# Optimization experiments

Hardware: AMD Instinct MI355X
Metric: run time of the kernel (lower is better)

Reference implementation:

```python
import jax, jax.numpy as jnp
import numpy as np

HEADS = 5 - 1  # 4 attention heads (GPSConv heads=4)


def _bn(x, g, b, eps=1e-5):
    # BatchNorm1d, training-mode math (biased variance), matches torch normalization
    mu = x.mean(0)
    var = x.var(0)
    return g * (x - mu) * jax.lax.rsqrt(var + eps) + b


def _forward(x, t, freqs, t_fc1_W, t_fc1_b, t_fc2_W, t_fc2_b, node_W, node_b,
             tproj_W, tproj_b, tcat_W, tcat_b, pen_g, pen_b, pel_W, pel_b,
             cat_W, cat_b, conv_Wg, gru_Wih, gru_bih, gru_Whh, gru_bhh,
             attn_Wqkv, attn_bqkv, attn_Wo, attn_bo, bn_g, bn_b,
             mlp_W1, mlp_b1, mlp_W2, mlp_b2, out_W, out_b):
    B, C, Hh, Ww = x.shape
    HD = node_W.shape[1]          # hidden_dim = 64
    DH = HD // HEADS              # per-head dim = 16
    WL = pen_g.shape[0]           # walk_length = 20

    xf = x.reshape(B, -1)                              # [B, D]
    h = xf @ node_W + node_b                           # node_proj

    # TimeEmbedding: t @ freqs -> sin/cos -> MLP, then time_proj
    tp = t.reshape(B, 1) * freqs.reshape(1, -1)        # [B, nf]
    two_pi = jnp.asarray(2.0 * np.pi, x.dtype)
    te = jnp.concatenate([jnp.sin(two_pi * tp), jnp.cos(two_pi * tp)], axis=-1)
    te = jax.nn.silu(te @ t_fc1_W + t_fc1_b) @ t_fc2_W + t_fc2_b
    h_time = te @ tproj_W + tproj_b
    h = jnp.concatenate([h, h_time], axis=-1) @ tcat_W + tcat_b  # time_cat_proj

    # Fully-connected graph incl. self-loops: A = 1 everywhere, deg = B.
    # Random-walk PE: P = A/deg has all entries 1/B; P is idempotent (P@P = P),
    # hence diag(P^k) = diag(P) = 1/B for every k in 1..walk_length.
    A = jnp.ones((B, B), x.dtype)
    P = A / A.sum(1, keepdims=True)
    pe = jnp.broadcast_to(jnp.diagonal(P)[:, None], (B, WL))
    pe = _bn(pe, pen_g, pen_b)                         # pe_norm (batch stats)
    h = jnp.concatenate([h, pe @ pel_W + pel_b], axis=-1) @ cat_W + cat_b

    inv_sqrt = jnp.asarray(1.0 / np.sqrt(DH), x.dtype)
    for l in range(conv_Wg.shape[0]):                  # 5 GPSConv layers
        # --- GatedGraphConv (num_layers=1): message, add-aggregate, GRU ---
        m = A @ (h @ conv_Wg[l])                       # sum of messages from all src nodes
        gi = m @ gru_Wih[l] + gru_bih[l]               # [B, 3H]
        gh = h @ gru_Whh[l] + gru_bhh[l]
        ir, iz, inn = jnp.split(gi, 3, axis=-1)
        hr, hz, hn = jnp.split(gh, 3, axis=-1)
        r = jax.nn.sigmoid(ir + hr)
        z = jax.nn.sigmoid(iz + hz)
        n = jnp.tanh(inn + r * hn)
        hc = (1.0 - z) * n + z * h                     # GRUCell output
        h1 = _bn(hc + h, bn_g[l, 0], bn_b[l, 0])       # residual + norm1

        # --- global multihead self-attention over the single dense batch ---
        qkv = h @ attn_Wqkv[l] + attn_bqkv[l]
        q, k, v = jnp.split(qkv, 3, axis=-1)
        q = q.reshape(B, HEADS, DH).transpose(1, 0, 2)  # [h, B, d]
        k = k.reshape(B, HEADS, DH).transpose(1, 0, 2)
        v = v.reshape(B, HEADS, DH).transpose(1, 0, 2)
        att = jax.nn.softmax(jnp.einsum('hqd,hkd->hqk', q, k) * inv_sqrt, axis=-1)
        o = jnp.einsum('hqk,hkd->hqd', att, v).transpose(1, 0, 2).reshape(B, HD)
        o = o @ attn_Wo[l] + attn_bo[l]
        h2 = _bn(o + h, bn_g[l, 1], bn_b[l, 1])        # residual + norm2

        s = h1 + h2
        s = s + (jax.nn.relu(s @ mlp_W1[l] + mlp_b1[l]) @ mlp_W2[l] + mlp_b2[l])
        h = _bn(s, bn_g[l, 2], bn_b[l, 2])             # norm3

    return (h @ out_W + out_b).reshape(B, C, Hh, Ww)


def setup_inputs() -> dict:
    key = jax.random.key(0)
    B, C, H, W = 2048, 4, 32, 32
    D = C * H * W                 # 4096
    HD, PE, WL, L = 64, 16, 20, 5
    NF, TH, TC = 8, 64, 64
    ks = iter(jax.random.split(key, 40))

    def rn(shape, s=0.05):
        return jax.random.normal(next(ks), shape, jnp.float32) * s

    return {
        'x': jax.random.normal(next(ks), (B, C, H, W), jnp.float32),
        't': jax.random.uniform(next(ks), (B,), jnp.float32),
        'freqs': rn((NF,), 1.0),
        't_fc1_W': rn((2 * NF, TH)), 't_fc1_b': rn((TH,)),
        't_fc2_W': rn((TH, TC)), 't_fc2_b': rn((TC,)),
        'node_W': rn((D, HD), 0.02), 'node_b': rn((HD,)),
        'tproj_W': rn((TC, HD)), 'tproj_b': rn((HD,)),
        'tcat_W': rn((2 * HD, HD)), 'tcat_b': rn((HD,)),
        'pen_g': jnp.ones((WL,), jnp.float32), 'pen_b': jnp.zeros((WL,), jnp.float32),
        'pel_W': rn((WL, PE)), 'pel_b': rn((PE,)),
        'cat_W': rn((HD + PE, HD)), 'cat_b': rn((HD,)),
        'conv_Wg': rn((L, HD, HD)),
        'gru_Wih': rn((L, HD, 3 * HD)), 'gru_bih': rn((L, 3 * HD)),
        'gru_Whh': rn((L, HD, 3 * HD)), 'gru_bhh': rn((L, 3 * HD)),
        'attn_Wqkv': rn((L, HD, 3 * HD)), 'attn_bqkv': rn((L, 3 * HD)),
        'attn_Wo': rn((L, HD, HD)), 'attn_bo': rn((L, HD)),
        'bn_g': jnp.ones((L, 3, HD), jnp.float32), 'bn_b': jnp.zeros((L, 3, HD), jnp.float32),
        'mlp_W1': rn((L, HD, 2 * HD)), 'mlp_b1': rn((L, 2 * HD)),
        'mlp_W2': rn((L, 2 * HD, HD)), 'mlp_b2': rn((L, HD)),
        'out_W': rn((HD, D)), 'out_b': rn((D,)),
    }


def reference(x, t, freqs, t_fc1_W, t_fc1_b, t_fc2_W, t_fc2_b, node_W, node_b,
              tproj_W, tproj_b, tcat_W, tcat_b, pen_g, pen_b, pel_W, pel_b,
              cat_W, cat_b, conv_Wg, gru_Wih, gru_bih, gru_Whh, gru_bhh,
              attn_Wqkv, attn_bqkv, attn_Wo, attn_bo, bn_g, bn_b,
              mlp_W1, mlp_b1, mlp_W2, mlp_b2, out_W, out_b):
    return _forward(x, t, freqs, t_fc1_W, t_fc1_b, t_fc2_W, t_fc2_b, node_W, node_b,
                    tproj_W, tproj_b, tcat_W, tcat_b, pen_g, pen_b, pel_W, pel_b,
                    cat_W, cat_b, conv_Wg, gru_Wih, gru_bih, gru_Whh, gru_bhh,
                    attn_Wqkv, attn_bqkv, attn_Wo, attn_bo, bn_g, bn_b,
                    mlp_W1, mlp_b1, mlp_W2, mlp_b2, out_W, out_b)
```

## Files before the change

kernel.cpp:

```cpp
#include <hip/hip_runtime.h>

#define NB 2048
#define HDM 64
#define NLAY 5

typedef __bf16 bf16x8 __attribute__((ext_vector_type(8)));
typedef float v4f __attribute__((ext_vector_type(4)));

__device__ __forceinline__ float sigmoidf_(float x){ return 1.f/(1.f+__expf(-x)); }
__device__ __forceinline__ float tanhfast_(float x){
  x = fminf(fmaxf(x, -15.f), 15.f);
  float e = __expf(2.f*x);
  return (e-1.f)/(e+1.f);
}
__device__ __forceinline__ unsigned short f2b_rne(float f){
  unsigned u = __float_as_uint(f);
  unsigned r = u + 0x7FFFu + ((u>>16)&1u);
  return (unsigned short)(r>>16);
}
__device__ __forceinline__ unsigned pk2(float a, float b){
  unsigned ua = (__float_as_uint(a) + 0x8000u) >> 16;
  unsigned ub = (__float_as_uint(b) + 0x8000u) & 0xFFFF0000u;
  return ua | ub;
}

__global__ __launch_bounds__(256) void k_pre(
    const float* __restrict__ x, const float* __restrict__ tt,
    const float* __restrict__ freqs,
    const float* __restrict__ fc1W, const float* __restrict__ fc1b,
    const float* __restrict__ fc2W, const float* __restrict__ fc2b,
    const float* __restrict__ tprojW, const float* __restrict__ tprojb,
    const float* __restrict__ nodeW,
    float* __restrict__ h0p, float* __restrict__ htime,
    float* __restrict__ zero_region)
{
  __shared__ float xs[16*256];
  __shared__ float tb0[256];
  __shared__ float tb1[256];
  const int t = threadIdx.x, blk = blockIdx.x;
  const int r = t>>6, c = t&63;

  if (blk == 0){
    for (int i = t; i < 320 + 1920; i += 256) zero_region[i] = 0.f;
  }

  {
    const int row = blk*4 + r;
    const float tv = tt[row];
    float te[16];
    #pragma unroll
    for (int j=0;j<8;++j){
      float sv, cv;
      __sincosf(6.28318530717958647692f*tv*freqs[j], &sv, &cv);
      te[j]=sv; te[j+8]=cv;
    }
    float a = fc1b[c];
    #pragma unroll
    for (int j=0;j<16;++j) a += te[j]*fc1W[j*64+c];
    tb0[t] = a*sigmoidf_(a);
    __syncthreads();
    float b2 = fc2b[c];
    for (int k=0;k<64;++k) b2 += tb0[r*64+k]*fc2W[k*64+c];
    tb1[t] = b2;
    __syncthreads();
    float hti = tprojb[c];
    for (int k=0;k<64;++k) hti += tb1[r*64+k]*tprojW[k*64+c];
    htime[row*64+c] = hti;
  }

  const int rg = blk>>2, kq = blk&3;
  const int rows0 = rg*16, k0 = kq*1024;
  const int cq = t&15, rr = t>>4;
  float4 acc; acc.x=0.f; acc.y=0.f; acc.z=0.f; acc.w=0.f;
  for (int ch=0; ch<4; ++ch){
    __syncthreads();
    const int kb = k0 + ch*256;
    #pragma unroll
    for (int i=0;i<4;++i){
      int fi = t + 256*i;
      int xr = fi>>6, kk = (fi&63)<<2;
      *(float4*)&xs[xr*256+kk] = *(const float4*)&x[(size_t)(rows0+xr)*4096 + kb + kk];
    }
    __syncthreads();
    #pragma unroll 4
    for (int k=0;k<256;++k){
      float4 w = *(const float4*)&nodeW[(size_t)(kb+k)*64 + 4*cq];
      float xv = xs[rr*256+k];
      acc.x += xv*w.x; acc.y += xv*w.y; acc.z += xv*w.z; acc.w += xv*w.w;
    }
  }
  *(float4*)&h0p[(size_t)kq*(NB*HDM) + (rows0+rr)*64 + 4*cq] = acc;
}

__global__ __launch_bounds__(256) void k_assemble(
    const float* __restrict__ h0p, const float* __restrict__ htime,
    const float* __restrict__ nodeb,
    const float* __restrict__ tcatW, const float* __restrict__ tcatb,
    const float* __restrict__ penb, const float* __restrict__ pelW,
    const float* __restrict__ pelb,
    const float* __restrict__ catW, const float* __restrict__ catb,
    float* __restrict__ hbuf)
{
  __shared__ float sa[256];
  __shared__ float sb[256];
  __shared__ float cvec[64];
  const int t = threadIdx.x, blk = blockIdx.x;
  const int r = t>>6, c = t&63;
  const int row = blk*4 + r;

  if (r==0){
    float pl[16];
    #pragma unroll
    for (int j=0;j<16;++j){
      float a = pelb[j];
      for (int w=0;w<20;++w) a += penb[w]*pelW[w*16+j];
      pl[j]=a;
    }
    float a = catb[c];
    #pragma unroll
    for (int j=0;j<16;++j) a += pl[j]*catW[(64+j)*64+c];
    cvec[c]=a;
  }
  float h0 = nodeb[c];
  #pragma unroll
  for (int q=0;q<4;++q) h0 += h0p[(size_t)q*(NB*HDM) + row*64 + c];
  sa[t] = h0;
  sb[t] = htime[row*64+c];
  __syncthreads();
  float a = tcatb[c];
  for (int k=0;k<64;++k) a += sa[r*64+k]*tcatW[k*64+c];
  for (int k=0;k<64;++k) a += sb[r*64+k]*tcatW[(64+k)*64+c];
  __syncthreads();
  sa[t] = a;
  __syncthreads();
  float hv = cvec[c];
  for (int k=0;k<64;++k) hv += sa[r*64+k]*catW[k*64+c];
  hbuf[row*64+c] = hv;
}

__global__ __launch_bounds__(256) void k_A(
    const float* __restrict__ smlp,
    const float* __restrict__ bnaccPrev,
    const float* __restrict__ gPrev, const float* __restrict__ bPrev,
    float* __restrict__ hbuf, float* __restrict__ hsumL,
    const float* __restrict__ Whh, const float* __restrict__ bhh,
    const float* __restrict__ Wq,  const float* __restrict__ bq,
    float* __restrict__ gh,
    unsigned short* __restrict__ Qb, unsigned short* __restrict__ Kb,
    unsigned short* __restrict__ Vt, int first)
{
  __shared__ float sa[256];
  const int t = threadIdx.x, blk = blockIdx.x;
  const int r = t>>6, c = t&63;
  const int row0 = blk*4;
  const int row = row0 + r;

  float hv;
  if (first){
    hv = hbuf[row*64+c];
  } else {
    float mu = bnaccPrev[256+c]*(1.f/NB);
    float va = bnaccPrev[320+c]*(1.f/NB) - mu*mu;
    hv = gPrev[c]*(smlp[row*64+c]-mu)*rsqrtf(va+1e-5f)+bPrev[c];
    hbuf[row*64+c] = hv;
  }
  sa[t] = hv;
  __syncthreads();
  if (t<64){
    atomicAdd(&hsumL[t], sa[t]+sa[64+t]+sa[128+t]+sa[192+t]);
  }
  #pragma unroll
  for (int i=0;i<3;++i){
    int idx = t + 256*i;
    int rr = idx/192, cc = idx - rr*192;
    float ag = bhh[cc], aq = bq[cc];
    for (int k=0;k<64;++k){
      float hk = sa[rr*64+k];
      ag += hk*Whh[k*192+cc];
      aq += hk*Wq[k*192+cc];
    }
    int rw = row0+rr;
    gh[(size_t)rw*192+cc] = ag;
    if (cc < 64){
      int hd = cc>>4, dh = cc&15;
      size_t base = ((size_t)(hd<<11) + rw)*32;
      Qb[base+dh] = f2b_rne(aq*0.25f);
      Qb[base+16+dh] = 0;
    } else if (cc < 128){
      int c2 = cc-64, hd = c2>>4, dh = c2&15;
      size_t base = ((size_t)(hd<<11) + rw)*32;
      Kb[base+dh] = f2b_rne(aq);
      Kb[base+16+dh] = 0;
    } else {
      int c2 = cc-128, hd = c2>>4, dh = c2&15;
      Vt[((size_t)(hd*16+dh))*2048 + rw] = f2b_rne(aq);
    }
  }
}

__global__ __launch_bounds__(64) void k_attn(
    const unsigned short* __restrict__ Qb, const unsigned short* __restrict__ Kb,
    const unsigned short* __restrict__ Vt,
    float* __restrict__ Upart, float* __restrict__ mpart, float* __restrict__ lpart)
{
  __shared__ unsigned short Pl[16*40];
  const int lane = threadIdx.x;
  const int q15 = lane & 15, quad = lane >> 4;
  const int b = blockIdx.x;
  const int qt = b & 127, head = (b>>7)&3, part = b>>9;
  const int qrow = qt*16 + q15;
  const int key00 = part*512;

  const bf16x8 qf = *(const bf16x8*)&Qb[(((size_t)(head<<11))+qrow)*32 + quad*8];
  const unsigned short* Kb_h = Kb + ((size_t)(head<<11))*32;
  const unsigned short* Vrow = Vt + ((size_t)(head*16+q15))*2048;

  v4f O = {0.f,0.f,0.f,0.f};
  float m = -1e30f, lsum = 0.f;

  bf16x8 kf0 = *(const bf16x8*)&Kb_h[(size_t)(key00 + q15)*32 + quad*8];
  bf16x8 kf1 = *(const bf16x8*)&Kb_h[(size_t)(key00 + 16 + q15)*32 + quad*8];
  bf16x8 vf  = *(const bf16x8*)&Vrow[key00 + quad*8];

  for (int c=0; c<16; ++c){
    bf16x8 nk0, nk1, nv;
    if (c < 15){
      int nk = key00 + (c+1)*32;
      nk0 = *(const bf16x8*)&Kb_h[(size_t)(nk + q15)*32 + quad*8];
      nk1 = *(const bf16x8*)&Kb_h[(size_t)(nk + 16 + q15)*32 + quad*8];
      nv  = *(const bf16x8*)&Vrow[nk + quad*8];
    }
    v4f z = {0.f,0.f,0.f,0.f};
    v4f s0 = __builtin_amdgcn_mfma_f32_16x16x32_bf16(kf0, qf, z, 0,0,0);
    v4f s1 = __builtin_amdgcn_mfma_f32_16x16x32_bf16(kf1, qf, z, 0,0,0);
    float cmax = fmaxf(fmaxf(fmaxf(s0[0],s0[1]),fmaxf(s0[2],s0[3])),
                       fmaxf(fmaxf(s1[0],s1[1]),fmaxf(s1[2],s1[3])));
    cmax = fmaxf(cmax, __shfl_xor(cmax,16,64));
    cmax = fmaxf(cmax, __shfl_xor(cmax,32,64));
    float mnew = fmaxf(m, cmax);
    float alpha = __expf(m - mnew);
    float p0=__expf(s0[0]-mnew), p1=__expf(s0[1]-mnew), p2=__expf(s0[2]-mnew), p3=__expf(s0[3]-mnew);
    float p4=__expf(s1[0]-mnew), p5=__expf(s1[1]-mnew), p6=__expf(s1[2]-mnew), p7=__expf(s1[3]-mnew);
    lsum = alpha*lsum + ((p0+p1)+(p2+p3)+((p4+p5)+(p6+p7)));
    m = mnew;
    O[0]*=alpha; O[1]*=alpha; O[2]*=alpha; O[3]*=alpha;
    *(uint2*)&Pl[q15*40 + quad*4]      = make_uint2(pk2(p0,p1), pk2(p2,p3));
    *(uint2*)&Pl[q15*40 + 16 + quad*4] = make_uint2(pk2(p4,p5), pk2(p6,p7));
    __syncthreads();
    bf16x8 pf = *(const bf16x8*)&Pl[q15*40 + quad*8];
    O = __builtin_amdgcn_mfma_f32_16x16x32_bf16(vf, pf, O, 0,0,0);
    kf0 = nk0; kf1 = nk1; vf = nv;
  }
  lsum += __shfl_xor(lsum,16,64);
  lsum += __shfl_xor(lsum,32,64);
  size_t ub = ((size_t)((part*4+head)*2048) + qrow)*16 + quad*4;
  *(float4*)&Upart[ub] = make_float4(O[0],O[1],O[2],O[3]);
  if (quad==0){
    mpart[(size_t)(part*4+head)*2048 + qrow] = m;
    lpart[(size_t)(part*4+head)*2048 + qrow] = lsum;
  }
}

__global__ __launch_bounds__(256) void k_B2(
    const float* __restrict__ hbuf, const float* __restrict__ gh,
    const float* __restrict__ hsumL,
    const float* __restrict__ Upart, const float* __restrict__ mpart,
    const float* __restrict__ lpart,
    const float* __restrict__ Wg,   const float* __restrict__ Wih,
    const float* __restrict__ bih,  const float* __restrict__ Wo,
    const float* __restrict__ bo,
    float* __restrict__ s1, float* __restrict__ s2, float* __restrict__ bnaccL)
{
  __shared__ float sa[256];
  __shared__ float os[256];
  __shared__ float smv_[64];
  __shared__ float sgi[192];
  __shared__ float Sb[512];
  const int t = threadIdx.x, blk = blockIdx.x;
  const int r = t>>6, c = t&63;
  const int row = blk*4 + r;
  const int head = c>>4, dh = c&15;

  if (t<64){
    float a=0.f;
    for (int k=0;k<64;++k) a += hsumL[k]*Wg[k*64+t];
    smv_[t]=a;
  }
  sa[t] = hbuf[row*64+c];

  float m0 = mpart[(size_t)(head)*2048+row],    m1 = mpart[(size_t)(4+head)*2048+row];
  float m2 = mpart[(size_t)(8+head)*2048+row],  m3 = mpart[(size_t)(12+head)*2048+row];
  float mm = fmaxf(fmaxf(m0,m1),fmaxf(m2,m3));
  float a0=__expf(m0-mm), a1=__expf(m1-mm), a2=__expf(m2-mm), a3=__expf(m3-mm);
  float ll = a0*lpart[(size_t)(head)*2048+row]   + a1*lpart[(size_t)(4+head)*2048+row]
           + a2*lpart[(size_t)(8+head)*2048+row] + a3*lpart[(size_t)(12+head)*2048+row];
  float uu = a0*Upart[((size_t)(head)*2048+row)*16+dh]    + a1*Upart[((size_t)(4+head)*2048+row)*16+dh]
           + a2*Upart[((size_t)(8+head)*2048+row)*16+dh]  + a3*Upart[((size_t)(12+head)*2048+row)*16+dh];
  os[t] = uu / ll;
  __syncthreads();
  if (t<192){
    float a = bih[t];
    for (int k=0;k<64;++k) a += smv_[k]*Wih[k*192+t];
    sgi[t]=a;
  }
  __syncthreads();

  float o2 = bo[c];
  for (int k=0;k<64;++k) o2 += os[r*64+k]*Wo[k*64+c];
  float hv = sa[t];
  float s2v = o2 + hv;
  float ir = sgi[c]      + gh[(size_t)row*192+c];
  float iz = sgi[64+c]   + gh[(size_t)row*192+64+c];
  float inn = sgi[128+c];
  float hn  = gh[(size_t)row*192+128+c];
  float rr_ = sigmoidf_(ir);
  float zz  = sigmoidf_(iz);
  float nn  = tanhfast_(inn + rr_*hn);
  float s1v = (1.f-zz)*nn + zz*hv + hv;
  s1[row*64+c] = s1v;
  s2[row*64+c] = s2v;
  Sb[t] = s1v; Sb[256+t] = s2v;
  __syncthreads();
  if (t<64){
    float a=0.f,aq=0.f,b=0.f,bq2=0.f;
    #pragma unroll
    for (int rr=0;rr<4;++rr){
      float v1 = Sb[rr*64+t], v2 = Sb[256+rr*64+t];
      a+=v1; aq+=v1*v1; b+=v2; bq2+=v2*v2;
    }
    atomicAdd(&bnaccL[t],a);     atomicAdd(&bnaccL[64+t],aq);
    atomicAdd(&bnaccL[128+t],b); atomicAdd(&bnaccL[192+t],bq2);
  }
}

__global__ __launch_bounds__(256) void k_C(
    const float* __restrict__ s1, const float* __restrict__ s2,
    const float* __restrict__ bngL, const float* __restrict__ bnbL,
    const float* __restrict__ W1, const float* __restrict__ b1,
    const float* __restrict__ W2, const float* __restrict__ b2,
    float* __restrict__ smlp, float* __restrict__ bnaccL)
{
  __shared__ float sa[256];
  __shared__ float sh[512];
  __shared__ float S2[256];
  const int t = threadIdx.x, blk = blockIdx.x;
  const int r = t>>6, c = t&63;
  const int row = blk*4 + r;

  float mu1 = bnaccL[c]*(1.f/NB);
  float va1 = bnaccL[64+c]*(1.f/NB) - mu1*mu1;
  float mu2 = bnaccL[128+c]*(1.f/NB);
  float va2 = bnaccL[192+c]*(1.f/NB) - mu2*mu2;
  float h1 = bngL[c]*(s1[row*64+c]-mu1)*rsqrtf(va1+1e-5f)+bnbL[c];
  float h2 = bngL[64+c]*(s2[row*64+c]-mu2)*rsqrtf(va2+1e-5f)+bnbL[64+c];
  float sv = h1+h2;
  sa[t]=sv;
  __syncthreads();
  #pragma unroll
  for (int i=0;i<2;++i){
    int idx = t + 256*i;
    int rr = idx>>7, hj = idx&127;
    float a = b1[hj];
    for (int k=0;k<64;++k) a += sa[rr*64+k]*W1[k*128+hj];
    sh[idx] = fmaxf(a, 0.f);
  }
  __syncthreads();
  float mo = b2[c];
  for (int k=0;k<128;++k) mo += sh[r*128+k]*W2[k*64+c];
  float smv2 = sv + mo;
  smlp[row*64+c]=smv2;
  S2[t]=smv2;
  __syncthreads();
  if (t<64){
    float a=0.f,aq=0.f;
    #pragma unroll
    for (int rr=0;rr<4;++rr){ float v=S2[rr*64+t]; a+=v; aq+=v*v; }
    atomicAdd(&bnaccL[256+t],a); atomicAdd(&bnaccL[320+t],aq);
  }
}

__global__ __launch_bounds__(256) void k_out(
  const float* __restrict__ smlp, const float* __restrict__ bnacc4,
  const float* __restrict__ g4, const float* __restrict__ b4,
  const float* __restrict__ outW, const float* __restrict__ outb,
  float* __restrict__ out)
{
  __shared__ float hsT[64*20];
  const int t = threadIdx.x, blk = blockIdx.x;
  const int rg = blk>>2, cg = blk&3;
  const int rows0 = rg*16;
  #pragma unroll
  for (int i=0;i<4;++i){
    int idx = t + 256*i;
    int k = idx&63, rr = idx>>6;
    float mu = bnacc4[256+k]*(1.f/NB);
    float va = bnacc4[320+k]*(1.f/NB)-mu*mu;
    hsT[k*20+rr] = g4[k]*(smlp[(size_t)(rows0+rr)*64+k]-mu)*rsqrtf(va+1e-5f)+b4[k];
  }
  __syncthreads();
  for (int j=0;j<4;++j){
    int cc = cg*1024 + t + 256*j;
    float acc[16];
    float bv = outb[cc];
    #pragma unroll
    for (int rr=0;rr<16;++rr) acc[rr]=bv;
    for (int k=0;k<64;++k){
      float w = outW[(size_t)k*4096+cc];
      const float4* hp = (const float4*)&hsT[k*20];
      float4 h0=hp[0], h1=hp[1], h2=hp[2], h3=hp[3];
      acc[0]+=h0.x*w;  acc[1]+=h0.y*w;  acc[2]+=h0.z*w;  acc[3]+=h0.w*w;
      acc[4]+=h1.x*w;  acc[5]+=h1.y*w;  acc[6]+=h1.z*w;  acc[7]+=h1.w*w;
      acc[8]+=h2.x*w;  acc[9]+=h2.y*w;  acc[10]+=h2.z*w; acc[11]+=h2.w*w;
      acc[12]+=h3.x*w; acc[13]+=h3.y*w; acc[14]+=h3.z*w; acc[15]+=h3.w*w;
    }
    #pragma unroll
    for (int rr=0;rr<16;++rr) out[(size_t)(rows0+rr)*4096+cc]=acc[rr];
  }
}

extern "C" void kernel_launch(void* const* d_in, const int* in_sizes, int n_in,
                              void* d_out, int out_size, void* d_ws, size_t ws_size,
                              hipStream_t stream)
{
  (void)in_sizes; (void)n_in; (void)out_size; (void)ws_size;
  const float* x      = (const float*)d_in[0];
  const float* tt     = (const float*)d_in[1];
  const float* freqs  = (const float*)d_in[2];
  const float* fc1W   = (const float*)d_in[3];
  const float* fc1b   = (const float*)d_in[4];
  const float* fc2W   = (const float*)d_in[5];
  const float* fc2b   = (const float*)d_in[6];
  const float* nodeW  = (const float*)d_in[7];
  const float* nodeb  = (const float*)d_in[8];
  const float* tprojW = (const float*)d_in[9];
  const float* tprojb = (const float*)d_in[10];
  const float* tcatW  = (const float*)d_in[11];
  const float* tcatb  = (const float*)d_in[12];
  const float* penb   = (const float*)d_in[14];
  const float* pelW   = (const float*)d_in[15];
  const float* pelb   = (const float*)d_in[16];
  const float* catW   = (const float*)d_in[17];
  const float* catb   = (const float*)d_in[18];
  const float* convWg = (const float*)d_in[19];
  const float* gruWih = (const float*)d_in[20];
  const float* grubih = (const float*)d_in[21];
  const float* gruWhh = (const float*)d_in[22];
  const float* grubhh = (const float*)d_in[23];
  const float* Wqkv   = (const float*)d_in[24];
  const float* bqkv   = (const float*)d_in[25];
  const float* Wo     = (const float*)d_in[26];
  const float* bo     = (const float*)d_in[27];
  const float* bng    = (const float*)d_in[28];
  const float* bnb    = (const float*)d_in[29];
  const float* W1     = (const float*)d_in[30];
  const float* b1     = (const float*)d_in[31];
  const float* W2     = (const float*)d_in[32];
  const float* b2     = (const float*)d_in[33];
  const float* outW   = (const float*)d_in[34];
  const float* outb   = (const float*)d_in[35];

  float* ws = (float*)d_ws;
  float* h0p   = ws;
  float* htime = h0p + 524288;
  float* hbuf  = htime + 131072;
  float* gh    = hbuf + 131072;
  float* s1    = gh + 393216;
  float* s2    = s1 + 131072;
  float* smlp  = s2 + 131072;
  float* Upart = smlp + 131072;
  float* mpart = Upart + 524288;
  float* lpart = mpart + 32768;
  float* hsum  = lpart + 32768;
  float* bnacc = hsum + 320;
  unsigned short* Qb = (unsigned short*)(bnacc + 1920);
  unsigned short* Kb = Qb + 262144;
  unsigned short* Vt = Kb + 262144;

  dim3 G(512), Blk(256);

  k_pre<<<G, Blk, 0, stream>>>(x, tt, freqs, fc1W, fc1b, fc2W, fc2b,
                               tprojW, tprojb, nodeW, h0p, htime, hsum);

  k_assemble<<<G, Blk, 0, stream>>>(h0p, htime, nodeb, tcatW, tcatb,
                                    penb, pelW, pelb, catW, catb, hbuf);

  for (int l=0; l<NLAY; ++l){
    const float* bnaccPrev = (l==0) ? bnacc : bnacc + (l-1)*384;
    const float* gPrev = (l==0) ? bng : bng + (l-1)*192 + 128;
    const float* bPrev = (l==0) ? bnb : bnb + (l-1)*192 + 128;
    k_A<<<G, Blk, 0, stream>>>(smlp, bnaccPrev, gPrev, bPrev,
                               hbuf, hsum + l*64,
                               gruWhh + l*12288, grubhh + l*192,
                               Wqkv + l*12288, bqkv + l*192,
                               gh, Qb, Kb, Vt, (l==0) ? 1 : 0);
    k_attn<<<dim3(2048), dim3(64), 0, stream>>>(Qb, Kb, Vt, Upart, mpart, lpart);
    k_B2<<<G, Blk, 0, stream>>>(hbuf, gh, hsum + l*64, Upart, mpart, lpart,
                                convWg + l*4096, gruWih + l*12288, grubih + l*192,
                                Wo + l*4096, bo + l*64,
                                s1, s2, bnacc + l*384);
    k_C<<<G, Blk, 0, stream>>>(s1, s2, bng + l*192, bnb + l*192,
                               W1 + l*8192, b1 + l*128, W2 + l*8192, b2 + l*64,
                               smlp, bnacc + l*384);
  }

  k_out<<<G, Blk, 0, stream>>>(smlp, bnacc + 4*384, bng + 896, bnb + 896,
                               outW, outb, (float*)d_out);
}
```

Measured before the change: 638.5 us.

## Register-tile node projection GEMM with 8-way K split and reuse attention buffer

The node projection in k_pre now runs on 1024 blocks with an 8-way K split. Each thread computes a 4x4 register tile from a transposed shared-memory x tile, and partial K slices are reduced in shared memory. This raises arithmetic intensity per weight load and exposes more parallelism, but k_assemble must sum 8 partial buffers instead of 4. The h0p scratch now aliases the attention Upart buffer, which must hold all 8 partials. Several small matmul loops in k_A, k_B2, the MLP and the output kernel are restructured or annotated with unroll pragmas to improve ILP.

```diff
diff --git a/kernel.cpp b/kernel.cpp
--- a/kernel.cpp
+++ b/kernel.cpp
@@ -34,9 +34,9 @@
     float* __restrict__ h0p, float* __restrict__ htime,
     float* __restrict__ zero_region)
 {
-  __shared__ float xs[16*256];
-  __shared__ float tb0[256];
-  __shared__ float tb1[256];
+  __shared__ float xsT[256*20];
+  __shared__ float tb0[128];
+  __shared__ float tb1[128];
   const int t = threadIdx.x, blk = blockIdx.x;
   const int r = t>>6, c = t&63;
 
@@ -45,51 +45,87 @@
   }
 
   {
-    const int row = blk*4 + r;
+    const int row = blk*2 + (r&1);
     const float tv = tt[row];
-    float te[16];
-    #pragma unroll
-    for (int j=0;j<8;++j){
-      float sv, cv;
-      __sincosf(6.28318530717958647692f*tv*freqs[j], &sv, &cv);
-      te[j]=sv; te[j+8]=cv;
-    }
-    float a = fc1b[c];
-    #pragma unroll
-    for (int j=0;j<16;++j) a += te[j]*fc1W[j*64+c];
-    tb0[t] = a*sigmoidf_(a);
+    if (r < 2){
+      float te[16];
+      #pragma unroll
+      for (int j=0;j<8;++j){
+        float sv, cv;
+        __sincosf(6.28318530717958647692f*tv*freqs[j], &sv, &cv);
+        te[j]=sv; te[j+8]=cv;
+      }
+      float a = fc1b[c];
+      #pragma unroll
+      for (int j=0;j<16;++j) a += te[j]*fc1W[j*64+c];
+      tb0[r*64+c] = a*sigmoidf_(a);
+    }
     __syncthreads();
-    float b2 = fc2b[c];
-    for (int k=0;k<64;++k) b2 += tb0[r*64+k]*fc2W[k*64+c];
-    tb1[t] = b2;
+    if (r < 2){
+      float b2 = fc2b[c];
+      #pragma unroll 8
+      for (int k=0;k<64;++k) b2 += tb0[r*64+k]*fc2W[k*64+c];
+      tb1[r*64+c] = b2;
+    }
     __syncthreads();
-    float hti = tprojb[c];
-    for (int k=0;k<64;++k) hti += tb1[r*64+k]*tprojW[k*64+c];
-    htime[row*64+c] = hti;
-  }
-
-  const int rg = blk>>2, kq = blk&3;
-  const int rows0 = rg*16, k0 = kq*1024;
-  const int cq = t&15, rr = t>>4;
-  float4 acc; acc.x=0.f; acc.y=0.f; acc.z=0.f; acc.w=0.f;
-  for (int ch=0; ch<4; ++ch){
+    if (r < 2){
+      float hti = tprojb[c];
+      #pragma unroll 8
+      for (int k=0;k<64;++k) hti += tb1[r*64+k]*tprojW[k*64+c];
+      htime[row*64+c] = hti;
+    }
+  }
+
+  const int rg = blk>>3, kq = blk&7;
+  const int rows0 = rg*16, k0 = kq*512;
+  const int col4 = (t&15)*4;
+  const int rq4  = ((t>>4)&3)*4;
+  const int ksub = (t>>6)*64;
+
+  float4 a0={0,0,0,0}, a1={0,0,0,0}, a2={0,0,0,0}, a3={0,0,0,0};
+
+  for (int ch=0; ch<2; ++ch){
     __syncthreads();
-    const int kb = k0 + ch*256;
     #pragma unroll
     for (int i=0;i<4;++i){
       int fi = t + 256*i;
       int xr = fi>>6, kk = (fi&63)<<2;
-      *(float4*)&xs[xr*256+kk] = *(const float4*)&x[(size_t)(rows0+xr)*4096 + kb + kk];
+      float4 xv = *(const float4*)&x[(size_t)(rows0+xr)*4096 + k0 + ch*256 + kk];
+      xsT[(kk+0)*20+xr]=xv.x; xsT[(kk+1)*20+xr]=xv.y;
+      xsT[(kk+2)*20+xr]=xv.z; xsT[(kk+3)*20+xr]=xv.w;
     }
     __syncthreads();
-    #pragma unroll 4
-    for (int k=0;k<256;++k){
-      float4 w = *(const float4*)&nodeW[(size_t)(kb+k)*64 + 4*cq];
-      float xv = xs[rr*256+k];
-      acc.x += xv*w.x; acc.y += xv*w.y; acc.z += xv*w.z; acc.w += xv*w.w;
-    }
-  }
-  *(float4*)&h0p[(size_t)kq*(NB*HDM) + (rows0+rr)*64 + 4*cq] = acc;
+    const float* wp = &nodeW[(size_t)(k0 + ch*256 + ksub)*64 + col4];
+    const float* xp = &xsT[ksub*20 + rq4];
+    #pragma unroll 8
+    for (int kk=0; kk<64; ++kk){
+      float4 w  = *(const float4*)&wp[kk*64];
+      float4 xr4 = *(const float4*)&xp[kk*20];
+      a0.x += xr4.x*w.x; a0.y += xr4.x*w.y; a0.z += xr4.x*w.z; a0.w += xr4.x*w.w;
+      a1.x += xr4.y*w.x; a1.y += xr4.y*w.y; a1.z += xr4.y*w.z; a1.w += xr4.y*w.w;
+      a2.x += xr4.z*w.x; a2.y += xr4.z*w.y; a2.z += xr4.z*w.z; a2.w += xr4.z*w.w;
+      a3.x += xr4.w*w.x; a3.y += xr4.w*w.y; a3.z += xr4.w*w.z; a3.w += xr4.w*w.w;
+    }
+  }
+  __syncthreads();
+  {
+    const int kqi = t>>6;
+    *(float4*)&xsT[(kqi*16 + rq4 + 0)*64 + col4] = a0;
+    *(float4*)&xsT[(kqi*16 + rq4 + 1)*64 + col4] = a1;
+    *(float4*)&xsT[(kqi*16 + rq4 + 2)*64 + col4] = a2;
+    *(float4*)&xsT[(kqi*16 + rq4 + 3)*64 + col4] = a3;
+  }
+  __syncthreads();
+  {
+    const int row = t>>4, c4 = (t&15)*4;
+    float4 s = {0,0,0,0};
+    #pragma unroll
+    for (int q=0;q<4;++q){
+      float4 v = *(const float4*)&xsT[(q*16+row)*64 + c4];
+      s.x+=v.x; s.y+=v.y; s.z+=v.z; s.w+=v.w;
+    }
+    *(float4*)&h0p[(size_t)kq*(NB*HDM) + (rows0+row)*64 + c4] = s;
+  }
 }
 
 __global__ __launch_bounds__(256) void k_assemble(
@@ -123,17 +159,21 @@
   }
   float h0 = nodeb[c];
   #pragma unroll
-  for (int q=0;q<4;++q) h0 += h0p[(size_t)q*(NB*HDM) + row*64 + c];
+  for (int q=0;q<8;++q) h0 += h0p[(size_t)q*(NB*HDM) + row*64 + c];
   sa[t] = h0;
   sb[t] = htime[row*64+c];
   __syncthreads();
   float a = tcatb[c];
-  for (int k=0;k<64;++k) a += sa[r*64+k]*tcatW[k*64+c];
-  for (int k=0;k<64;++k) a += sb[r*64+k]*tcatW[(64+k)*64+c];
+  #pragma unroll 4
+  for (int k=0;k<64;++k){
+    a += sa[r*64+k]*tcatW[k*64+c];
+    a += sb[r*64+k]*tcatW[(64+k)*64+c];
+  }
   __syncthreads();
   sa[t] = a;
   __syncthreads();
   float hv = cvec[c];
+  #pragma unroll 8
   for (int k=0;k<64;++k) hv += sa[r*64+k]*catW[k*64+c];
   hbuf[row*64+c] = hv;
 }
@@ -169,31 +209,41 @@
   if (t<64){
     atomicAdd(&hsumL[t], sa[t]+sa[64+t]+sa[128+t]+sa[192+t]);
   }
+  int rrA[3], ccA[3];
+  float ag[3], aq[3];
   #pragma unroll
   for (int i=0;i<3;++i){
     int idx = t + 256*i;
-    int rr = idx/192, cc = idx - rr*192;
-    float ag = bhh[cc], aq = bq[cc];
-    for (int k=0;k<64;++k){
-      float hk = sa[rr*64+k];
-      ag += hk*Whh[k*192+cc];
-      aq += hk*Wq[k*192+cc];
-    }
-    int rw = row0+rr;
-    gh[(size_t)rw*192+cc] = ag;
+    rrA[i] = idx/192; ccA[i] = idx - rrA[i]*192;
+    ag[i] = bhh[ccA[i]]; aq[i] = bq[ccA[i]];
+  }
+  #pragma unroll 4
+  for (int k=0;k<64;++k){
+    #pragma unroll
+    for (int i=0;i<3;++i){
+      float hk = sa[rrA[i]*64+k];
+      ag[i] += hk*Whh[k*192+ccA[i]];
+      aq[i] += hk*Wq [k*192+ccA[i]];
+    }
+  }
+  #pragma unroll
+  for (int i=0;i<3;++i){
+    int rw = row0 + rrA[i], cc = ccA[i];
+    gh[(size_t)rw*192+cc] = ag[i];
+    float aqv = aq[i];
     if (cc < 64){
       int hd = cc>>4, dh = cc&15;
       size_t base = ((size_t)(hd<<11) + rw)*32;
-      Qb[base+dh] = f2b_rne(aq*0.25f);
+      Qb[base+dh] = f2b_rne(aqv*0.25f);
       Qb[base+16+dh] = 0;
     } else if (cc < 128){
       int c2 = cc-64, hd = c2>>4, dh = c2&15;
       size_t base = ((size_t)(hd<<11) + rw)*32;
-      Kb[base+dh] = f2b_rne(aq);
+      Kb[base+dh] = f2b_rne(aqv);
       Kb[base+16+dh] = 0;
     } else {
       int c2 = cc-128, hd = c2>>4, dh = c2&15;
-      Vt[((size_t)(hd*16+dh))*2048 + rw] = f2b_rne(aq);
+      Vt[((size_t)(hd*16+dh))*2048 + rw] = f2b_rne(aqv);
     }
   }
 }
@@ -283,6 +333,7 @@
 
   if (t<64){
     float a=0.f;
+    #pragma unroll 8
     for (int k=0;k<64;++k) a += hsumL[k]*Wg[k*64+t];
     smv_[t]=a;
   }
@@ -300,12 +351,14 @@
   __syncthreads();
   if (t<192){
     float a = bih[t];
+    #pragma unroll 8
     for (int k=0;k<64;++k) a += smv_[k]*Wih[k*192+t];
     sgi[t]=a;
   }
   __syncthreads();
 
   float o2 = bo[c];
+  #pragma unroll 8
   for (int k=0;k<64;++k) o2 += os[r*64+k]*Wo[k*64+c];
   float hv = sa[t];
   float s2v = o2 + hv;
@@ -356,16 +409,22 @@
   float sv = h1+h2;
   sa[t]=sv;
   __syncthreads();
-  #pragma unroll
-  for (int i=0;i<2;++i){
-    int idx = t + 256*i;
-    int rr = idx>>7, hj = idx&127;
-    float a = b1[hj];
-    for (int k=0;k<64;++k) a += sa[rr*64+k]*W1[k*128+hj];
-    sh[idx] = fmaxf(a, 0.f);
+  {
+    const int rr0 = t>>7, hj0 = t&127;
+    const int idx1 = t + 256;
+    const int rr1 = idx1>>7, hj1 = idx1&127;
+    float a0v = b1[hj0], a1v = b1[hj1];
+    #pragma unroll 4
+    for (int k=0;k<64;++k){
+      a0v += sa[rr0*64+k]*W1[k*128+hj0];
+      a1v += sa[rr1*64+k]*W1[k*128+hj1];
+    }
+    sh[t] = fmaxf(a0v, 0.f);
+    sh[t+256] = fmaxf(a1v, 0.f);
   }
   __syncthreads();
   float mo = b2[c];
+  #pragma unroll 8
   for (int k=0;k<128;++k) mo += sh[r*128+k]*W2[k*64+c];
   float smv2 = sv + mo;
   smlp[row*64+c]=smv2;
@@ -404,6 +463,7 @@
     float bv = outb[cc];
     #pragma unroll
     for (int rr=0;rr<16;++rr) acc[rr]=bv;
+    #pragma unroll 4
     for (int k=0;k<64;++k){
       float w = outW[(size_t)k*4096+cc];
       const float4* hp = (const float4*)&hsT[k*20];
@@ -460,26 +520,26 @@
   const float* outb   = (const float*)d_in[35];
 
   float* ws = (float*)d_ws;
-  float* h0p   = ws;
-  float* htime = h0p + 524288;
+  float* htime = ws;
   float* hbuf  = htime + 131072;
   float* gh    = hbuf + 131072;
   float* s1    = gh + 393216;
   float* s2    = s1 + 131072;
   float* smlp  = s2 + 131072;
-  float* Upart = smlp + 131072;
+  float* hsum  = smlp + 131072;
+  float* bnacc = hsum + 320;
+  float* Upart = bnacc + 1920;
   float* mpart = Upart + 524288;
   float* lpart = mpart + 32768;
-  float* hsum  = lpart + 32768;
-  float* bnacc = hsum + 320;
-  unsigned short* Qb = (unsigned short*)(bnacc + 1920);
+  unsigned short* Qb = (unsigned short*)(lpart + 32768);
   unsigned short* Kb = Qb + 262144;
   unsigned short* Vt = Kb + 262144;
+  float* h0p = Upart;
 
   dim3 G(512), Blk(256);
 
-  k_pre<<<G, Blk, 0, stream>>>(x, tt, freqs, fc1W, fc1b, fc2W, fc2b,
-                               tprojW, tprojb, nodeW, h0p, htime, hsum);
+  k_pre<<<dim3(1024), Blk, 0, stream>>>(x, tt, freqs, fc1W, fc1b, fc2W, fc2b,
+                                        tprojW, tprojb, nodeW, h0p, htime, hsum);
 
   k_assemble<<<G, Blk, 0, stream>>>(h0p, htime, nodeb, tcatW, tcatb,
                                     penb, pelW, pelb, catW, catb, hbuf);
```

After: 612.1 us. 4.1% less time.
